# Kernel optimization log

Hardware: AMD Instinct MI355X
Metric: run time of the kernel (lower is better)

Reference implementation:

```python
import jax, jax.numpy as jnp
import numpy as np

EPS = 1e-5
NH = 8   # num_heads
P = 8    # patch_size (local window)

def layernorm(x, g, b):
    m = jnp.mean(x, axis=-1, keepdims=True)
    v = jnp.var(x, axis=-1, keepdims=True)
    return (x - m) * jax.lax.rsqrt(v + EPS) * g + b

def axis_embed(pos, nf):
    # DETR-style interleaved sin/cos along one axis -> (L, nf)
    dim_t = 10000.0 ** (2.0 * (jnp.arange(nf) // 2).astype(jnp.float32) / nf)
    p = pos[:, None] / dim_t
    return jnp.stack([jnp.sin(p[:, 0::2]), jnp.cos(p[:, 1::2])], axis=-1).reshape(pos.shape[0], nf)

def pos_embed_2d(E, H, W):
    # (H, W, E): first half of channels encode y, second half encode x
    half = E // 2
    ye = axis_embed(jnp.arange(1, H + 1, dtype=jnp.float32), half)
    xe = axis_embed(jnp.arange(1, W + 1, dtype=jnp.float32), half)
    return jnp.concatenate([jnp.broadcast_to(ye[:, None, :], (H, W, half)),
                            jnp.broadcast_to(xe[None, :, :], (H, W, half))], axis=-1)

def pos_embed_1d(L, E):
    # standard sinusoidal, (L, 1, E)
    pos = jnp.arange(L, dtype=jnp.float32)[:, None]
    div = jnp.exp(jnp.arange(0, E, 2, dtype=jnp.float32) * (-np.log(10000.0) / E))
    pe = jnp.zeros((L, E), jnp.float32)
    pe = pe.at[:, 0::2].set(jnp.sin(pos * div)).at[:, 1::2].set(jnp.cos(pos * div))
    return pe[:, None, :]

def mha(q, k, v, Wq, bq, Wk, bk, Wv, bv, Wo, bo, nh):
    # q,k,v: (B, L, C)
    B, Lq, C = q.shape
    hd = C // nh
    qh = (q @ Wq + bq).reshape(B, Lq, nh, hd)
    kh = (k @ Wk + bk).reshape(B, -1, nh, hd)
    vh = (v @ Wv + bv).reshape(B, -1, nh, hd)
    att = jax.nn.softmax(jnp.einsum('bqhd,bkhd->bhqk', qh, kh) / np.sqrt(hd).astype(np.float32), axis=-1)
    out = jnp.einsum('bhqk,bkhd->bqhd', att, vh).reshape(B, Lq, C)
    return out @ Wo + bo

def win_part(x):
    # (N,T,H,W,C) -> (N*T*nWin, P*P, C)
    N, T, H, W, C = x.shape
    x = x.reshape(N, T, H // P, P, W // P, P, C).transpose(0, 1, 2, 4, 3, 5, 6)
    return x.reshape(-1, P * P, C)

def forward(x, g1, b1, g2, b2, g3, b3, g4, b4,
            sWq, sbq, sWk, sbk, sWv, sbv, sWo, sbo,
            cW1, cb1, dwk, dwb, cW2, cb2,
            tWq, tbq, tWk, tbk, tWv, tbv, tWo, tbo,
            fW1, fb1, fW2, fb2):
    N, T, H, W, C = x.shape
    sl_pos = jnp.tile(pos_embed_2d(C, P, P), (H // P, W // P, 1))  # (H,W,C)
    tem_pos = pos_embed_1d(T, C)                                   # (T,1,C)

    # --- spatial local windowed MHSA (q=k=norm1(x+pos), v=norm1(x)) ---
    qk = win_part(layernorm(x + sl_pos, g1, b1))
    vv = win_part(layernorm(x, g1, b1))
    attn = mha(qk, qk, vv, sWq, sbq, sWk, sbk, sWv, sbv, sWo, sbo, NH)
    attn = attn.reshape(N, T, H // P, W // P, P, P, C).transpose(0, 1, 2, 4, 3, 5, 6).reshape(N, T, H, W, C)
    x = x + attn

    # --- Conv FFN: linear -> depthwise 3x3 -> GELU -> linear ---
    h = layernorm(x, g2, b2) @ cW1 + cb1
    Ch = h.shape[-1]
    h = h.reshape(N * T, H, W, Ch).transpose(0, 3, 1, 2)  # NCHW
    h = jax.lax.conv_general_dilated(h, dwk, (1, 1), 'SAME', feature_group_count=Ch,
                                     dimension_numbers=('NCHW', 'OIHW', 'NCHW')) + dwb[None, :, None, None]
    h = jax.nn.gelu(h, approximate=False)
    h = h.transpose(0, 2, 3, 1).reshape(N, T, H, W, Ch)
    x = x + (h @ cW2 + cb2)

    # --- temporal MHSA over T, tokens are (n,h,w) positions ---
    xt = x.transpose(1, 0, 2, 3, 4).reshape(T, N * H * W, C)
    xt = layernorm(xt, g3, b3)
    qt = layernorm(xt + tem_pos, g3, b3).transpose(1, 0, 2)  # (B,T,C)
    vt = layernorm(xt, g3, b3).transpose(1, 0, 2)
    xt = xt + mha(qt, qt, vt, tWq, tbq, tWk, tbk, tWv, tbv, tWo, tbo, NH).transpose(1, 0, 2)

    # --- FFN; original does x = x + drop3(x) (no residual, doubles output) ---
    xt = layernorm(xt, g4, b4)
    xt = jax.nn.gelu(xt @ fW1 + fb1, approximate=False) @ fW2 + fb2
    xt = xt + xt
    return xt.reshape(T, N, H, W, C).transpose(1, 0, 2, 3, 4)

def setup_inputs() -> dict:
    key = jax.random.key(0)
    N, T, H, W, C, DFF, HID = 4, 16, 32, 32, 256, 1024, 1024
    ks = iter(jax.random.split(key, 64))
    def w(*s):
        return jax.random.normal(next(ks), s, jnp.float32) * 0.02
    inp = dict(x=jax.random.normal(next(ks), (N, T, H, W, C), jnp.float32))
    for i in ('1', '2', '3', '4'):
        inp['g' + i] = jnp.ones((C,), jnp.float32)
        inp['b' + i] = jnp.zeros((C,), jnp.float32)
    for pfx in ('s', 't'):
        inp.update({pfx + 'Wq': w(C, C), pfx + 'bq': jnp.zeros((C,), jnp.float32),
                    pfx + 'Wk': w(C, C), pfx + 'bk': jnp.zeros((C,), jnp.float32),
                    pfx + 'Wv': w(C, C), pfx + 'bv': jnp.zeros((C,), jnp.float32),
                    pfx + 'Wo': w(C, C), pfx + 'bo': jnp.zeros((C,), jnp.float32)})
    inp.update(cW1=w(C, HID), cb1=jnp.zeros((HID,), jnp.float32),
               dwk=w(HID, 1, 3, 3), dwb=jnp.zeros((HID,), jnp.float32),
               cW2=w(HID, C), cb2=jnp.zeros((C,), jnp.float32))
    inp.update(fW1=w(C, DFF), fb1=jnp.zeros((DFF,), jnp.float32),
               fW2=w(DFF, C), fb2=jnp.zeros((C,), jnp.float32))
    return inp

def reference(x, g1, b1, g2, b2, g3, b3, g4, b4,
              sWq, sbq, sWk, sbk, sWv, sbv, sWo, sbo,
              cW1, cb1, dwk, dwb, cW2, cb2,
              tWq, tbq, tWk, tbk, tWv, tbv, tWo, tbo,
              fW1, fb1, fW2, fb2):
    return forward(x, g1, b1, g2, b2, g3, b3, g4, b4,
                   sWq, sbq, sWk, sbk, sWv, sbv, sWo, sbo,
                   cW1, cb1, dwk, dwb, cW2, cb2,
                   tWq, tbq, tWk, tbk, tWv, tbv, tWo, tbo,
                   fW1, fb1, fW2, fb2)
```

## Files before the change

kernel.cpp:

```cpp
#include <hip/hip_runtime.h>
#include <hip/hip_bf16.h>

typedef unsigned short u16;
typedef unsigned int u32;
typedef __attribute__((ext_vector_type(4))) float f32x4;
typedef __attribute__((ext_vector_type(8))) short s16x8;

static constexpr int Nn = 4, Tt = 16, Hh = 32, Ww = 32, Cc = 256;
static constexpr int Ltok = Nn * Tt * Hh * Ww;

__device__ __forceinline__ float bf2f(u16 v) {
  union { u32 u; float f; } t; t.u = ((u32)v) << 16; return t.f;
}
__device__ __forceinline__ u16 f2bf(float f) {
  union { u32 u; float f; } t; t.f = f;
  return (u16)((t.u + 0x7fffu + ((t.u >> 16) & 1u)) >> 16);
}
__device__ __forceinline__ ushort4 pack4(float a, float b, float c, float d) {
  ushort4 r; r.x = f2bf(a); r.y = f2bf(b); r.z = f2bf(c); r.w = f2bf(d); return r;
}
__device__ __forceinline__ float geluf(float x) {
  return 0.5f * x * (1.0f + erff(x * 0.70710678118654752f));
}
__device__ __forceinline__ float wsum(float v) {
#pragma unroll
  for (int o = 32; o > 0; o >>= 1) v += __shfl_xor(v, o, 64);
  return v;
}
__device__ __forceinline__ void ln_stats(float a0, float a1, float a2, float a3,
                                         float& m, float& inv) {
  float s  = wsum(a0 + a1 + a2 + a3);
  float s2 = wsum(a0 * a0 + a1 * a1 + a2 * a2 + a3 * a3);
  m = s * (1.0f / 256.0f);
  float v = s2 * (1.0f / 256.0f) - m * m;
  inv = rsqrtf(v + 1e-5f);
}
__device__ __forceinline__ void gload16(const u16* g, u16* l) {
  __builtin_amdgcn_global_load_lds(
      (const __attribute__((address_space(1))) void*)g,
      (__attribute__((address_space(3))) void*)l, 16, 0, 0);
}

__global__ __launch_bounds__(256) void k_pos(float* __restrict__ pe2d,
                                             float* __restrict__ pe1d,
                                             float* __restrict__ dwkT,
                                             float* __restrict__ zb,
                                             const float* __restrict__ dwk) {
  int idx = blockIdx.x * 256 + threadIdx.x;
  if (idx < 16384) {
    int y = idx >> 11, r = idx & 2047, x = r >> 8, c = r & 255;
    float pos; int cc;
    if (c < 128) { pos = (float)(y + 1); cc = c; }
    else         { pos = (float)(x + 1); cc = c - 128; }
    float e = (float)(cc & ~1) * (1.0f / 128.0f);
    float v = pos / powf(10000.0f, e);
    pe2d[idx] = (cc & 1) ? cosf(v) : sinf(v);
  } else if (idx < 20480) {
    int i = idx - 16384;
    int t = i >> 8, c = i & 255;
    float e = (float)(c & ~1) * (1.0f / 256.0f);
    float v = (float)t * powf(10000.0f, -e);
    pe1d[i] = (c & 1) ? cosf(v) : sinf(v);
  } else if (idx < 29696) {
    int i = idx - 20480;
    int c = i & 1023, tap = i >> 10;
    dwkT[tap * 1024 + c] = dwk[c * 9 + tap];
  } else if (idx < 30720) {
    zb[idx - 29696] = 0.0f;
  }
}

__global__ __launch_bounds__(256) void k_wprep(
    const float* __restrict__ s0, const float* __restrict__ s1,
    const float* __restrict__ s2, const float* __restrict__ s3,
    const float* __restrict__ s4, const float* __restrict__ s5,
    const float* __restrict__ s6, const float* __restrict__ s7,
    const float* __restrict__ cW1, const float* __restrict__ cW2,
    const float* __restrict__ fW1, const float* __restrict__ fW2,
    u16* __restrict__ WT) {
  __shared__ float Ls[32][33];
  int b = blockIdx.x;
  const float* src; u16* dst; int Kd, Nd, tb;
  if (b < 512) {
    int seg = b >> 6; tb = b & 63; Kd = 256; Nd = 256;
    const float* tab[8] = {s0, s1, s2, s3, s4, s5, s6, s7};
    src = tab[seg]; dst = WT + seg * 65536;
  } else if (b < 768)  { tb = b - 512;  Kd = 256;  Nd = 1024; src = cW1; dst = WT + 524288; }
  else if (b < 1024)   { tb = b - 768;  Kd = 1024; Nd = 256;  src = cW2; dst = WT + 786432; }
  else if (b < 1280)   { tb = b - 1024; Kd = 256;  Nd = 1024; src = fW1; dst = WT + 1048576; }
  else                 { tb = b - 1280; Kd = 1024; Nd = 256;  src = fW2; dst = WT + 1310720; }
  int nt = Nd >> 5;
  int tk = tb / nt, tn = tb % nt;
  int r = threadIdx.x >> 3, c0 = (threadIdx.x & 7) * 4;
  float4 v = *(const float4*)&src[(size_t)(tk * 32 + r) * Nd + tn * 32 + c0];
  Ls[r][c0] = v.x; Ls[r][c0 + 1] = v.y; Ls[r][c0 + 2] = v.z; Ls[r][c0 + 3] = v.w;
  __syncthreads();
  *(ushort4*)&dst[(size_t)(tn * 32 + r) * Kd + tk * 32 + c0] =
      pack4(Ls[c0][r], Ls[c0 + 1][r], Ls[c0 + 2][r], Ls[c0 + 3][r]);
}

__global__ __launch_bounds__(256) void k_ln1(const float* __restrict__ x,
                                             const float* __restrict__ g,
                                             const float* __restrict__ b,
                                             const float* __restrict__ pe2d,
                                             u16* __restrict__ qk,
                                             u16* __restrict__ vv) {
  int l = blockIdx.x * 4 + (threadIdx.x >> 6);
  int lane = threadIdx.x & 63, c0 = lane * 4;
  int idx = l & 1023, hh = idx >> 5, ww = idx & 31;
  float4 xv = *(const float4*)&x[(size_t)l * Cc + c0];
  float4 pv = *(const float4*)&pe2d[(((hh & 7) << 3) | (ww & 7)) * Cc + c0];
  float q0 = xv.x + pv.x, q1 = xv.y + pv.y, q2 = xv.z + pv.z, q3 = xv.w + pv.w;
  float mx, ix, mq, iq;
  ln_stats(xv.x, xv.y, xv.z, xv.w, mx, ix);
  ln_stats(q0, q1, q2, q3, mq, iq);
  float4 gv = *(const float4*)&g[c0];
  float4 bv = *(const float4*)&b[c0];
  *(ushort4*)&qk[(size_t)l * Cc + c0] =
      pack4((q0 - mq) * iq * gv.x + bv.x, (q1 - mq) * iq * gv.y + bv.y,
            (q2 - mq) * iq * gv.z + bv.z, (q3 - mq) * iq * gv.w + bv.w);
  *(ushort4*)&vv[(size_t)l * Cc + c0] =
      pack4((xv.x - mx) * ix * gv.x + bv.x, (xv.y - mx) * ix * gv.y + bv.y,
            (xv.z - mx) * ix * gv.z + bv.z, (xv.w - mx) * ix * gv.w + bv.w);
}

__global__ __launch_bounds__(256) void k_lnb(const u16* __restrict__ x,
                                             const float* __restrict__ g,
                                             const float* __restrict__ b,
                                             u16* __restrict__ out) {
  int l = blockIdx.x * 4 + (threadIdx.x >> 6);
  int lane = threadIdx.x & 63, c0 = lane * 4;
  ushort4 xv4 = *(const ushort4*)&x[(size_t)l * Cc + c0];
  float x0 = bf2f(xv4.x), x1 = bf2f(xv4.y), x2 = bf2f(xv4.z), x3 = bf2f(xv4.w);
  float m, inv;
  ln_stats(x0, x1, x2, x3, m, inv);
  float4 gv = *(const float4*)&g[c0];
  float4 bv = *(const float4*)&b[c0];
  *(ushort4*)&out[(size_t)l * Cc + c0] =
      pack4((x0 - m) * inv * gv.x + bv.x, (x1 - m) * inv * gv.y + bv.y,
            (x2 - m) * inv * gv.z + bv.z, (x3 - m) * inv * gv.w + bv.w);
}

__global__ __launch_bounds__(256) void k_ln3b(const u16* __restrict__ xa,
                                              const float* __restrict__ g,
                                              const float* __restrict__ b,
                                              const float* __restrict__ pe1d,
                                              u16* __restrict__ xt_base,
                                              u16* __restrict__ qt,
                                              u16* __restrict__ vt) {
  int l = blockIdx.x * 4 + (threadIdx.x >> 6);
  int lane = threadIdx.x & 63, c0 = lane * 4;
  ushort4 xv4 = *(const ushort4*)&xa[(size_t)l * Cc + c0];
  float x0 = bf2f(xv4.x), x1 = bf2f(xv4.y), x2 = bf2f(xv4.z), x3 = bf2f(xv4.w);
  float4 gv = *(const float4*)&g[c0];
  float4 bv = *(const float4*)&b[c0];
  float m, inv;
  ln_stats(x0, x1, x2, x3, m, inv);
  float t0 = (x0 - m) * inv * gv.x + bv.x;
  float t1 = (x1 - m) * inv * gv.y + bv.y;
  float t2 = (x2 - m) * inv * gv.z + bv.z;
  float t3 = (x3 - m) * inv * gv.w + bv.w;
  *(ushort4*)&xt_base[(size_t)l * Cc + c0] = pack4(t0, t1, t2, t3);
  float m2, inv2;
  ln_stats(t0, t1, t2, t3, m2, inv2);
  *(ushort4*)&vt[(size_t)l * Cc + c0] =
      pack4((t0 - m2) * inv2 * gv.x + bv.x, (t1 - m2) * inv2 * gv.y + bv.y,
            (t2 - m2) * inv2 * gv.z + bv.z, (t3 - m2) * inv2 * gv.w + bv.w);
  int tt = (l >> 10) & 15;
  float4 pv = *(const float4*)&pe1d[tt * Cc + c0];
  float s0 = t0 + pv.x, s1 = t1 + pv.y, s2 = t2 + pv.z, s3 = t3 + pv.w;
  float m3, inv3;
  ln_stats(s0, s1, s2, s3, m3, inv3);
  *(ushort4*)&qt[(size_t)l * Cc + c0] =
      pack4((s0 - m3) * inv3 * gv.x + bv.x, (s1 - m3) * inv3 * gv.y + bv.y,
            (s2 - m3) * inv3 * gv.z + bv.z, (s3 - m3) * inv3 * gv.w + bv.w);
}

template <int MODE>
__global__ __launch_bounds__(256, 2) void k_sgemm(const u16* __restrict__ A,
                                                  const u16* __restrict__ WT,
                                                  const float* __restrict__ bias,
                                                  const void* __restrict__ res,
                                                  void* __restrict__ out,
                                                  int ldout) {
  __shared__ u16 SMEM[32768];
  const int tid = threadIdx.x;
  const int wave = tid >> 6, lane = tid & 63;
  const int fr = lane & 15, fs = lane >> 4;
  const int r0base = blockIdx.x * 128;
  s16x8 wreg[4][8];
#pragma unroll
  for (int ni = 0; ni < 4; ++ni)
#pragma unroll
    for (int kt = 0; kt < 8; ++kt)
      wreg[ni][kt] = *(const s16x8*)&WT[(size_t)(wave * 64 + ni * 16 + fr) * 256 +
                                        kt * 32 + fs * 8];
  auto stage = [&](int buf, int r0) {
    u16* Ad = SMEM + buf * 8192;
#pragma unroll
    for (int i = 0; i < 4; ++i) {
      int idx = i * 256 + tid;
      int row = idx >> 5, s = idx & 31;
      gload16(A + (size_t)(r0 + row) * 256 + ((s ^ row) << 3), &Ad[idx * 8]);
    }
  };
  float* sc = (float*)(SMEM + 16384) + wave * 2048;
  stage(0, r0base);
  __syncthreads();
#pragma unroll 1
  for (int c = 0; c < 4; ++c) {
    if (c < 3) stage((c + 1) & 1, r0base + (c + 1) * 32);
    const u16* As = SMEM + (c & 1) * 8192;
    f32x4 acc[2][4] = {};
#pragma unroll
    for (int kt = 0; kt < 8; ++kt) {
      s16x8 a0 = *(const s16x8*)&As[(fr * 32 + ((kt * 4 + fs) ^ fr)) * 8];
      s16x8 a1 = *(const s16x8*)&As[((16 + fr) * 32 + ((kt * 4 + fs) ^ (16 + fr))) * 8];
#pragma unroll
      for (int ni = 0; ni < 4; ++ni) {
        acc[0][ni] = __builtin_amdgcn_mfma_f32_16x16x32_bf16(a0, wreg[ni][kt],
                                                             acc[0][ni], 0, 0, 0);
        acc[1][ni] = __builtin_amdgcn_mfma_f32_16x16x32_bf16(a1, wreg[ni][kt],
                                                             acc[1][ni], 0, 0, 0);
      }
    }
    const int r0 = r0base + c * 32;
    if constexpr (MODE == 5) {
      u16* o = (u16*)out;
#pragma unroll
      for (int ni = 0; ni < 4; ++ni) {
        int gc = wave * 64 + ni * 16 + fr;
        float bv = bias[gc];
#pragma unroll
        for (int mi = 0; mi < 2; ++mi) {
          int gr = r0 + mi * 16 + fs * 4;
          *(ushort4*)&o[(size_t)gc * (size_t)Ltok + gr] =
              pack4(acc[mi][ni][0] + bv, acc[mi][ni][1] + bv,
                    acc[mi][ni][2] + bv, acc[mi][ni][3] + bv);
        }
      }
    } else {
#pragma unroll
      for (int mi = 0; mi < 2; ++mi)
#pragma unroll
        for (int ni = 0; ni < 4; ++ni)
#pragma unroll
          for (int r = 0; r < 4; ++r) {
            int row = mi * 16 + fs * 4 + r;
            int col = ni * 16 + fr;
            sc[row * 64 + (col ^ ((row & 7) << 3))] = acc[mi][ni][r];
          }
#pragma unroll
      for (int p = 0; p < 8; ++p) {
        int row = p * 4 + (lane >> 4);
        int c4 = (lane & 15) * 4;
        f32x4 v4 = *(const f32x4*)&sc[row * 64 + (c4 ^ ((row & 7) << 3))];
        int gr = r0 + row;
        int gc = wave * 64 + c4;
        float4 bv4 = *(const float4*)&bias[gc];
        float v[4] = {v4[0] + bv4.x, v4[1] + bv4.y, v4[2] + bv4.z, v4[3] + bv4.w};
        size_t o = (size_t)gr * (size_t)ldout + gc;
        if constexpr (MODE == 1) {
#pragma unroll
          for (int j = 0; j < 4; ++j) v[j] = geluf(v[j]);
        }
        if constexpr (MODE == 3) {
          ushort4 r4 = *(const ushort4*)&((const u16*)res)[(size_t)gr * 256 + gc];
          v[0] += bf2f(r4.x); v[1] += bf2f(r4.y); v[2] += bf2f(r4.z); v[3] += bf2f(r4.w);
        }
        if constexpr (MODE == 7) {
          float4 r4 = *(const float4*)&((const float*)res)[(size_t)gr * 256 + gc];
          v[0] += r4.x; v[1] += r4.y; v[2] += r4.z; v[3] += r4.w;
        }
        *(ushort4*)&((u16*)out)[o] = pack4(v[0], v[1], v[2], v[3]);
      }
    }
    __syncthreads();
  }
}

template <int MODE>
__global__ __launch_bounds__(256, 2) void k_m2(const u16* __restrict__ A,
                                               const u16* __restrict__ BT, int ldbt,
                                               const float* __restrict__ bias,
                                               const void* __restrict__ res,
                                               void* __restrict__ out, int K) {
  __shared__ u16 SMEM[16384];
  const int tid = threadIdx.x;
  const int wave = tid >> 6, lane = tid & 63;
  const int fr = lane & 15, fs = lane >> 4;
  const int m0 = blockIdx.x * 128, n0 = blockIdx.y * 64;
  const int wm = wave >> 1, wn = wave & 1;
  f32x4 acc[4][2] = {};

  auto stage = [&](int buf, int k0) {
    u16* Ad = SMEM + buf * 6144;
    u16* Bd = Ad + 4096;
#pragma unroll
    for (int i = 0; i < 2; ++i) {
      int idx = i * 256 + tid;
      int row = idx >> 2, s = idx & 3;
      gload16(A + (size_t)(m0 + row) * K + k0 + ((s ^ (row & 3)) << 3), &Ad[idx * 8]);
    }
    {
      int row = tid >> 2, s = tid & 3;
      gload16(BT + (size_t)(n0 + row) * ldbt + k0 + ((s ^ (row & 3)) << 3),
              &Bd[tid * 8]);
    }
  };
  auto compute = [&](int buf) {
    const u16* As = SMEM + buf * 6144;
    const u16* Bs = As + 4096;
    s16x8 af[4], bfr[2];
#pragma unroll
    for (int i = 0; i < 4; ++i) {
      int ra = wm * 64 + i * 16 + fr;
      af[i] = *(const s16x8*)&As[ra * 32 + ((fs ^ (ra & 3)) << 3)];
    }
#pragma unroll
    for (int j = 0; j < 2; ++j) {
      int rb = wn * 32 + j * 16 + fr;
      bfr[j] = *(const s16x8*)&Bs[rb * 32 + ((fs ^ (rb & 3)) << 3)];
    }
#pragma unroll
    for (int mi = 0; mi < 4; ++mi)
#pragma unroll
      for (int nj = 0; nj < 2; ++nj)
        acc[mi][nj] = __builtin_amdgcn_mfma_f32_16x16x32_bf16(af[mi], bfr[nj],
                                                              acc[mi][nj], 0, 0, 0);
  };

  stage(0, 0);
  __syncthreads();
  const int nt = K >> 5;
  int cur = 0;
  for (int t = 0; t < nt; ++t) {
    if (t < nt - 1) stage(cur ^ 1, (t + 1) << 5);
    compute(cur);
    __syncthreads();
    cur ^= 1;
  }
  float* Wl = (float*)SMEM + wave * 2048;
#pragma unroll
  for (int nj = 0; nj < 2; ++nj)
#pragma unroll
    for (int mi = 0; mi < 4; ++mi)
#pragma unroll
      for (int r = 0; r < 4; ++r) {
        int row = mi * 16 + fs * 4 + r;
        int col = nj * 16 + fr;
        Wl[row * 32 + (col ^ ((row & 7) << 2))] = acc[mi][nj][r];
      }
#pragma unroll
  for (int p = 0; p < 8; ++p) {
    int row = p * 8 + (lane >> 3);
    int c4 = (lane & 7) * 4;
    f32x4 v4 = *(const f32x4*)&Wl[row * 32 + (c4 ^ ((row & 7) << 2))];
    int gr = m0 + wm * 64 + row;
    int gc = n0 + wn * 32 + c4;
    float4 bv4 = *(const float4*)&bias[gc];
    float v[4] = {v4[0] + bv4.x, v4[1] + bv4.y, v4[2] + bv4.z, v4[3] + bv4.w};
    size_t o = (size_t)gr * 256 + gc;
    if constexpr (MODE == 3) {
      ushort4 r4 = *(const ushort4*)&((const u16*)res)[o];
      v[0] += bf2f(r4.x); v[1] += bf2f(r4.y); v[2] += bf2f(r4.z); v[3] += bf2f(r4.w);
      *(ushort4*)&((u16*)out)[o] = pack4(v[0], v[1], v[2], v[3]);
    } else {
      *(float4*)&((float*)out)[o] =
          make_float4(v[0] * 2.0f, v[1] * 2.0f, v[2] * 2.0f, v[3] * 2.0f);
    }
  }
}

__global__ __launch_bounds__(256) void k_sattn2(const u16* __restrict__ Q,
                                                const u16* __restrict__ Kb,
                                                const u16* __restrict__ VT,
                                                u16* __restrict__ ctx) {
  __shared__ u16 P_lds[4][4096];
  const int tid = threadIdx.x;
  const int wave = tid >> 6, lane = tid & 63;
  const int fr = lane & 15, fs = lane >> 4;
  const int wi = blockIdx.x >> 1;
  const int head = (blockIdx.x & 1) * 4 + wave;
  const int ft = wi >> 4, wy = (wi >> 2) & 3, wx = wi & 3;
  const int base = ft * 1024 + wy * 256 + wx * 8;
  const float scale = 0.17677669529663688f;
  const int ch = head * 32 + fs * 8;
  s16x8 ka[4], qb[4];
#pragma unroll
  for (int t4 = 0; t4 < 4; ++t4) {
    int tok = base + (2 * t4 + (fr >> 3)) * 32 + (fr & 7);
    ka[t4] = *(const s16x8*)&Kb[(size_t)tok * 256 + ch];
    qb[t4] = *(const s16x8*)&Q[(size_t)tok * 256 + ch];
  }
  f32x4 s[4][4] = {};
#pragma unroll
  for (int kt = 0; kt < 4; ++kt)
#pragma unroll
    for (int qt = 0; qt < 4; ++qt)
      s[kt][qt] = __builtin_amdgcn_mfma_f32_16x16x32_bf16(ka[kt], qb[qt], s[kt][qt], 0, 0, 0);
  u16* pw = P_lds[wave];
#pragma unroll
  for (int qt = 0; qt < 4; ++qt) {
    float m = -1e30f;
#pragma unroll
    for (int kt = 0; kt < 4; ++kt)
#pragma unroll
      for (int r = 0; r < 4; ++r) m = fmaxf(m, s[kt][qt][r]);
    m = fmaxf(m, __shfl_xor(m, 16, 64));
    m = fmaxf(m, __shfl_xor(m, 32, 64));
    m *= scale;
    float e[4][4];
    float sum = 0.f;
#pragma unroll
    for (int kt = 0; kt < 4; ++kt)
#pragma unroll
      for (int r = 0; r < 4; ++r) {
        e[kt][r] = __expf(s[kt][qt][r] * scale - m);
        sum += e[kt][r];
      }
    sum += __shfl_xor(sum, 16, 64);
    sum += __shfl_xor(sum, 32, 64);
    float il = 1.0f / sum;
    int q = qt * 16 + fr;
    int rowb = q * 128, sw = (q & 7) << 4;
#pragma unroll
    for (int kt = 0; kt < 4; ++kt)
      *(ushort4*)((char*)pw + ((rowb + kt * 32 + fs * 8) ^ sw)) =
          pack4(e[kt][0] * il, e[kt][1] * il, e[kt][2] * il, e[kt][3] * il);
  }
  f32x4 o[4][2] = {};
#pragma unroll
  for (int ks = 0; ks < 2; ++ks) {
    s16x8 vb[2];
#pragma unroll
    for (int nt = 0; nt < 2; ++nt) {
      int d = head * 32 + nt * 16 + fr;
      int tok = base + (ks * 4 + fs) * 32;
      vb[nt] = *(const s16x8*)&VT[(size_t)d * (size_t)Ltok + tok];
    }
#pragma unroll
    for (int qt = 0; qt < 4; ++qt) {
      int q = qt * 16 + fr;
      s16x8 pa = *(const s16x8*)((char*)pw +
                                 ((q * 128 + ks * 64 + fs * 16) ^ ((q & 7) << 4)));
#pragma unroll
      for (int nt = 0; nt < 2; ++nt)
        o[qt][nt] = __builtin_amdgcn_mfma_f32_16x16x32_bf16(pa, vb[nt], o[qt][nt], 0, 0, 0);
    }
  }
#pragma unroll
  for (int qt = 0; qt < 4; ++qt)
#pragma unroll
    for (int r = 0; r < 4; ++r) {
      int q = qt * 16 + fs * 4 + r;
      int tok = base + (q >> 3) * 32 + (q & 7);
#pragma unroll
      for (int nt = 0; nt < 2; ++nt)
        ctx[(size_t)tok * 256 + head * 32 + nt * 16 + fr] = f2bf(o[qt][nt][r]);
    }
}

__global__ __launch_bounds__(256) void k_tattn2(const u16* __restrict__ Q,
                                                const u16* __restrict__ Kb,
                                                const u16* __restrict__ V,
                                                u16* __restrict__ ctx) {
  __shared__ u16 Vs[16 * 256];
  const int tid = threadIdx.x;
  const int b = blockIdx.x;
  const int n = b >> 10, hw = b & 1023;
  const int tok0 = n * 16384 + hw;
#pragma unroll
  for (int i = 0; i < 2; ++i) {
    int chunk = tid * 2 + i;
    int row = chunk >> 5, c8 = (chunk & 31) * 8;
    *(uint4*)&Vs[row * 256 + c8] =
        *(const uint4*)&V[(size_t)(tok0 + row * 1024) * 256 + c8];
  }
  __syncthreads();
  const int wave = tid >> 6, lane = tid & 63;
  const int fr = lane & 15, fs = lane >> 4;
  const float scale = 0.17677669529663688f;
#pragma unroll
  for (int hg = 0; hg < 2; ++hg) {
    int head = wave + hg * 4;
    int ch = head * 32 + fs * 8;
    size_t go = (size_t)(tok0 + fr * 1024) * 256 + ch;
    s16x8 ka = *(const s16x8*)&Kb[go];
    s16x8 qb = *(const s16x8*)&Q[go];
    f32x4 s = {0.f, 0.f, 0.f, 0.f};
    s = __builtin_amdgcn_mfma_f32_16x16x32_bf16(ka, qb, s, 0, 0, 0);
    float m = fmaxf(fmaxf(s[0], s[1]), fmaxf(s[2], s[3]));
    m = fmaxf(m, __shfl_xor(m, 16, 64));
    m = fmaxf(m, __shfl_xor(m, 32, 64));
    m *= scale;
    float e0 = __expf(s[0] * scale - m), e1 = __expf(s[1] * scale - m);
    float e2 = __expf(s[2] * scale - m), e3 = __expf(s[3] * scale - m);
    float sum = e0 + e1 + e2 + e3;
    sum += __shfl_xor(sum, 16, 64);
    sum += __shfl_xor(sum, 32, 64);
    float il = 1.0f / sum;
    e0 *= il; e1 *= il; e2 *= il; e3 *= il;
    float o[8] = {};
#pragma unroll
    for (int kb = 0; kb < 4; ++kb) {
      int src = kb * 16 + fr;
      float p0 = __shfl(e0, src, 64);
      float p1 = __shfl(e1, src, 64);
      float p2 = __shfl(e2, src, 64);
      float p3 = __shfl(e3, src, 64);
#pragma unroll
      for (int r = 0; r < 4; ++r) {
        float p = r == 0 ? p0 : (r == 1 ? p1 : (r == 2 ? p2 : p3));
        uint4 vv = *(const uint4*)&Vs[(kb * 4 + r) * 256 + ch];
        const u16* vp = (const u16*)&vv;
#pragma unroll
        for (int u = 0; u < 8; ++u) o[u] = fmaf(p, bf2f(vp[u]), o[u]);
      }
    }
    size_t co = (size_t)(tok0 + fr * 1024) * 256 + ch;
    *(ushort4*)&ctx[co] = pack4(o[0], o[1], o[2], o[3]);
    *(ushort4*)&ctx[co + 4] = pack4(o[4], o[5], o[6], o[7]);
  }
}

__global__ __launch_bounds__(256) void k_dwconv(const u16* __restrict__ Hin,
                                                const float* __restrict__ dwkT,
                                                const float* __restrict__ dwb,
                                                int ch0, int oco,
                                                u16* __restrict__ Hout) {
  int flat = blockIdx.x * 256 + threadIdx.x;
  int l = flat >> 5, cg = flat & 31, c0 = cg * 8, tc0 = ch0 + c0;
  int frame = l >> 10, idx = l & 1023, hh = idx >> 5, ww = idx & 31;
  float acc[8];
  *(float4*)&acc[0] = *(const float4*)&dwb[tc0];
  *(float4*)&acc[4] = *(const float4*)&dwb[tc0 + 4];
#pragma unroll
  for (int ky = -1; ky <= 1; ++ky) {
    int h2 = hh + ky;
    if (h2 < 0 || h2 >= 32) continue;
#pragma unroll
    for (int kx = -1; kx <= 1; ++kx) {
      int w2 = ww + kx;
      if (w2 < 0 || w2 >= 32) continue;
      int ln = frame * 1024 + h2 * 32 + w2;
      uint4 hv = *(const uint4*)&Hin[(size_t)ln * 256 + c0];
      const u16* hp = (const u16*)&hv;
      int tap = (ky + 1) * 3 + (kx + 1);
      float wk[8];
      *(float4*)&wk[0] = *(const float4*)&dwkT[tap * 1024 + tc0];
      *(float4*)&wk[4] = *(const float4*)&dwkT[tap * 1024 + tc0 + 4];
#pragma unroll
      for (int u = 0; u < 8; ++u) acc[u] = fmaf(bf2f(hp[u]), wk[u], acc[u]);
    }
  }
  size_t ob = (size_t)l * 512 + oco + c0;
  *(ushort4*)&Hout[ob] = pack4(geluf(acc[0]), geluf(acc[1]), geluf(acc[2]), geluf(acc[3]));
  *(ushort4*)&Hout[ob + 4] = pack4(geluf(acc[4]), geluf(acc[5]), geluf(acc[6]), geluf(acc[7]));
}

extern "C" void kernel_launch(void* const* d_in, const int* in_sizes, int n_in,
                              void* d_out, int out_size, void* d_ws, size_t ws_size,
                              hipStream_t stream) {
  (void)in_sizes; (void)n_in; (void)out_size; (void)ws_size;
  const float* x   = (const float*)d_in[0];
  const float* g1  = (const float*)d_in[1];  const float* b1  = (const float*)d_in[2];
  const float* g2  = (const float*)d_in[3];  const float* b2  = (const float*)d_in[4];
  const float* g3  = (const float*)d_in[5];  const float* b3  = (const float*)d_in[6];
  const float* g4  = (const float*)d_in[7];  const float* b4  = (const float*)d_in[8];
  const float* sWq = (const float*)d_in[9];  const float* sbq = (const float*)d_in[10];
  const float* sWk = (const float*)d_in[11]; const float* sbk = (const float*)d_in[12];
  const float* sWv = (const float*)d_in[13]; const float* sbv = (const float*)d_in[14];
  const float* sWo = (const float*)d_in[15]; const float* sbo = (const float*)d_in[16];
  const float* tWq = (const float*)d_in[17]; const float* tbq = (const float*)d_in[18];
  const float* tWk = (const float*)d_in[19]; const float* tbk = (const float*)d_in[20];
  const float* tWv = (const float*)d_in[21]; const float* tbv = (const float*)d_in[22];
  const float* tWo = (const float*)d_in[23]; const float* tbo = (const float*)d_in[24];
  const float* cW1 = (const float*)d_in[25]; const float* cb1 = (const float*)d_in[26];
  const float* dwk = (const float*)d_in[27]; const float* dwb = (const float*)d_in[28];
  const float* cW2 = (const float*)d_in[29]; const float* cb2 = (const float*)d_in[30];
  const float* fW1 = (const float*)d_in[31]; const float* fb1 = (const float*)d_in[32];
  const float* fW2 = (const float*)d_in[33]; const float* fb2 = (const float*)d_in[34];

  char* ws = (char*)d_ws;
  const size_t MB = 1ull << 20;
  float* PE2D = (float*)(ws);
  float* PE1D = (float*)(ws + (64 << 10));
  float* DWKT = (float*)(ws + (80 << 10));
  float* ZB   = (float*)(ws + (116 << 10));
  u16*   WT   = (u16*)(ws + (128 << 10));
  u16* XA  = (u16*)(ws + 4 * MB);
  u16* X1  = (u16*)(ws + 4 * MB);
  u16* B1  = (u16*)(ws + 68 * MB);
  u16* B2  = (u16*)(ws + 100 * MB);
  u16* B3  = (u16*)(ws + 132 * MB);
  u16* B4  = (u16*)(ws + 164 * MB);
  u16* F1  = (u16*)(ws + 4 * MB);
  u16* H1q = B2;
  u16* H2h = B3;

  u16* sWqT = WT;               u16* sWkT = WT + 65536;
  u16* sWvT = WT + 2 * 65536;   u16* sWoT = WT + 3 * 65536;
  u16* tWqT = WT + 4 * 65536;   u16* tWkT = WT + 5 * 65536;
  u16* tWvT = WT + 6 * 65536;   u16* tWoT = WT + 7 * 65536;
  u16* cW1T = WT + 524288;      u16* cW2T = WT + 786432;
  u16* fW1T = WT + 1048576;     u16* fW2T = WT + 1310720;

  dim3 blk(256);
  dim3 gLN(Ltok / 4);
  dim3 gS(512);
  dim3 gM2(512, 4);

  k_pos<<<dim3(120), blk, 0, stream>>>(PE2D, PE1D, DWKT, ZB, dwk);
  k_wprep<<<dim3(1536), blk, 0, stream>>>(sWq, sWk, sWv, sWo, tWq, tWk, tWv, tWo,
                                          cW1, cW2, fW1, fW2, WT);
  k_ln1<<<gLN, blk, 0, stream>>>(x, g1, b1, PE2D, B1, B2);
  k_sgemm<5><<<gS, blk, 0, stream>>>(B2, sWvT, sbv, nullptr, B3, 0);
  k_sgemm<0><<<gS, blk, 0, stream>>>(B1, sWqT, sbq, nullptr, B2, 256);
  k_sgemm<0><<<gS, blk, 0, stream>>>(B1, sWkT, sbk, nullptr, B4, 256);
  k_sattn2<<<dim3(2048), blk, 0, stream>>>(B2, B4, B3, B1);
  k_sgemm<7><<<gS, blk, 0, stream>>>(B1, sWoT, sbo, x, XA, 256);
  k_lnb<<<gLN, blk, 0, stream>>>(XA, g2, b2, B1);
  for (int h = 0; h < 2; ++h) {
    for (int qq = 0; qq < 2; ++qq) {
      int q = h * 2 + qq;
      k_sgemm<0><<<gS, blk, 0, stream>>>(B1, cW1T + q * 65536, cb1 + q * 256,
                                         nullptr, H1q, 256);
      k_dwconv<<<dim3(Ltok * 32 / 256), blk, 0, stream>>>(H1q, DWKT, dwb,
                                                          q * 256, qq * 256, H2h);
    }
    k_m2<3><<<gM2, blk, 0, stream>>>(H2h, cW2T + h * 512, 1024,
                                     h ? cb2 : ZB, XA, XA, 512);
  }
  k_ln3b<<<gLN, blk, 0, stream>>>(XA, g3, b3, PE1D, B1, B2, B3);
  k_sgemm<0><<<gS, blk, 0, stream>>>(B3, tWvT, tbv, nullptr, B4, 256);
  k_sgemm<0><<<gS, blk, 0, stream>>>(B2, tWqT, tbq, nullptr, X1, 256);
  k_sgemm<0><<<gS, blk, 0, stream>>>(B2, tWkT, tbk, nullptr, B3, 256);
  k_tattn2<<<dim3(4096), blk, 0, stream>>>(X1, B3, B4, B2);
  k_sgemm<3><<<gS, blk, 0, stream>>>(B2, tWoT, tbo, B1, B3, 256);
  k_lnb<<<gLN, blk, 0, stream>>>(B3, g4, b4, B4);
  for (int q = 0; q < 4; ++q)
    k_sgemm<1><<<gS, blk, 0, stream>>>(B4, fW1T + q * 65536, fb1 + q * 256,
                                       nullptr, F1 + q * 256, 1024);
  k_m2<4><<<gM2, blk, 0, stream>>>(F1, fW2T, 1024, fb2, nullptr,
                                   (float*)d_out, 1024);
}
```

Before: 792.8 us.

## Widen k_m2 tile to 128x128 and stage transposed MODE 5 stores through LDS

```diff
diff --git a/kernel.cpp b/kernel.cpp
--- a/kernel.cpp
+++ b/kernel.cpp
@@ -205,6 +205,7 @@
     }
   };
   float* sc = (float*)(SMEM + 16384) + wave * 2048;
+  u16* sc2 = SMEM + 16384 + wave * 2048;
   stage(0, r0base);
   __syncthreads();
 #pragma unroll 1
@@ -229,15 +230,23 @@
       u16* o = (u16*)out;
 #pragma unroll
       for (int ni = 0; ni < 4; ++ni) {
-        int gc = wave * 64 + ni * 16 + fr;
-        float bv = bias[gc];
-#pragma unroll
-        for (int mi = 0; mi < 2; ++mi) {
-          int gr = r0 + mi * 16 + fs * 4;
-          *(ushort4*)&o[(size_t)gc * (size_t)Ltok + gr] =
-              pack4(acc[mi][ni][0] + bv, acc[mi][ni][1] + bv,
-                    acc[mi][ni][2] + bv, acc[mi][ni][3] + bv);
-        }
+        float bv = bias[wave * 64 + ni * 16 + fr];
+#pragma unroll
+        for (int mi = 0; mi < 2; ++mi)
+#pragma unroll
+          for (int r = 0; r < 4; ++r) {
+            int row = mi * 16 + fs * 4 + r;
+            int col = ni * 16 + fr;
+            sc2[col * 32 + row] = f2bf(acc[mi][ni][r] + bv);
+          }
+      }
+#pragma unroll
+      for (int p = 0; p < 4; ++p) {
+        int gcl = p * 16 + (lane >> 2);
+        int sub = lane & 3;
+        uint4 u = *(const uint4*)&sc2[gcl * 32 + sub * 8];
+        int gc = wave * 64 + gcl;
+        *(uint4*)&o[(size_t)gc * (size_t)Ltok + r0 + sub * 8] = u;
       }
     } else {
 #pragma unroll
@@ -289,45 +298,40 @@
   const int tid = threadIdx.x;
   const int wave = tid >> 6, lane = tid & 63;
   const int fr = lane & 15, fs = lane >> 4;
-  const int m0 = blockIdx.x * 128, n0 = blockIdx.y * 64;
+  const int bid = blockIdx.x;
+  const int m0 = (bid >> 1) * 128, n0 = (bid & 1) * 128;
   const int wm = wave >> 1, wn = wave & 1;
-  f32x4 acc[4][2] = {};
+  f32x4 acc[4][4] = {};
 
   auto stage = [&](int buf, int k0) {
-    u16* Ad = SMEM + buf * 6144;
+    u16* Ad = SMEM + buf * 8192;
     u16* Bd = Ad + 4096;
 #pragma unroll
     for (int i = 0; i < 2; ++i) {
       int idx = i * 256 + tid;
       int row = idx >> 2, s = idx & 3;
       gload16(A + (size_t)(m0 + row) * K + k0 + ((s ^ (row & 3)) << 3), &Ad[idx * 8]);
-    }
-    {
-      int row = tid >> 2, s = tid & 3;
       gload16(BT + (size_t)(n0 + row) * ldbt + k0 + ((s ^ (row & 3)) << 3),
-              &Bd[tid * 8]);
+              &Bd[idx * 8]);
     }
   };
   auto compute = [&](int buf) {
-    const u16* As = SMEM + buf * 6144;
+    const u16* As = SMEM + buf * 8192;
     const u16* Bs = As + 4096;
-    s16x8 af[4], bfr[2];
+    s16x8 af[4], bfr[4];
 #pragma unroll
     for (int i = 0; i < 4; ++i) {
       int ra = wm * 64 + i * 16 + fr;
       af[i] = *(const s16x8*)&As[ra * 32 + ((fs ^ (ra & 3)) << 3)];
-    }
-#pragma unroll
-    for (int j = 0; j < 2; ++j) {
-      int rb = wn * 32 + j * 16 + fr;
-      bfr[j] = *(const s16x8*)&Bs[rb * 32 + ((fs ^ (rb & 3)) << 3)];
+      int rb = wn * 64 + i * 16 + fr;
+      bfr[i] = *(const s16x8*)&Bs[rb * 32 + ((fs ^ (rb & 3)) << 3)];
     }
 #pragma unroll
     for (int mi = 0; mi < 4; ++mi)
 #pragma unroll
-      for (int nj = 0; nj < 2; ++nj)
-        acc[mi][nj] = __builtin_amdgcn_mfma_f32_16x16x32_bf16(af[mi], bfr[nj],
-                                                              acc[mi][nj], 0, 0, 0);
+      for (int ni = 0; ni < 4; ++ni)
+        acc[mi][ni] = __builtin_amdgcn_mfma_f32_16x16x32_bf16(af[mi], bfr[ni],
+                                                              acc[mi][ni], 0, 0, 0);
   };
 
   stage(0, 0);
@@ -342,33 +346,39 @@
   }
   float* Wl = (float*)SMEM + wave * 2048;
 #pragma unroll
-  for (int nj = 0; nj < 2; ++nj)
+  for (int nh = 0; nh < 2; ++nh) {
 #pragma unroll
     for (int mi = 0; mi < 4; ++mi)
 #pragma unroll
-      for (int r = 0; r < 4; ++r) {
-        int row = mi * 16 + fs * 4 + r;
-        int col = nj * 16 + fr;
-        Wl[row * 32 + (col ^ ((row & 7) << 2))] = acc[mi][nj][r];
-      }
-#pragma unroll
-  for (int p = 0; p < 8; ++p) {
-    int row = p * 8 + (lane >> 3);
-    int c4 = (lane & 7) * 4;
-    f32x4 v4 = *(const f32x4*)&Wl[row * 32 + (c4 ^ ((row & 7) << 2))];
-    int gr = m0 + wm * 64 + row;
-    int gc = n0 + wn * 32 + c4;
-    float4 bv4 = *(const float4*)&bias[gc];
-    float v[4] = {v4[0] + bv4.x, v4[1] + bv4.y, v4[2] + bv4.z, v4[3] + bv4.w};
-    size_t o = (size_t)gr * 256 + gc;
-    if constexpr (MODE == 3) {
-      ushort4 r4 = *(const ushort4*)&((const u16*)res)[o];
-      v[0] += bf2f(r4.x); v[1] += bf2f(r4.y); v[2] += bf2f(r4.z); v[3] += bf2f(r4.w);
-      *(ushort4*)&((u16*)out)[o] = pack4(v[0], v[1], v[2], v[3]);
-    } else {
-      *(float4*)&((float*)out)[o] =
-          make_float4(v[0] * 2.0f, v[1] * 2.0f, v[2] * 2.0f, v[3] * 2.0f);
-    }
+      for (int nq = 0; nq < 2; ++nq) {
+        int ni = nh * 2 + nq;
+#pragma unroll
+        for (int r = 0; r < 4; ++r) {
+          int row = mi * 16 + fs * 4 + r;
+          int col = nq * 16 + fr;
+          Wl[row * 32 + (col ^ ((row & 7) << 2))] = acc[mi][ni][r];
+        }
+      }
+#pragma unroll
+    for (int p = 0; p < 8; ++p) {
+      int row = p * 8 + (lane >> 3);
+      int c4 = (lane & 7) * 4;
+      f32x4 v4 = *(const f32x4*)&Wl[row * 32 + (c4 ^ ((row & 7) << 2))];
+      int gr = m0 + wm * 64 + row;
+      int gc = n0 + wn * 64 + nh * 32 + c4;
+      float4 bv4 = *(const float4*)&bias[gc];
+      float v[4] = {v4[0] + bv4.x, v4[1] + bv4.y, v4[2] + bv4.z, v4[3] + bv4.w};
+      size_t o = (size_t)gr * 256 + gc;
+      if constexpr (MODE == 3) {
+        ushort4 r4 = *(const ushort4*)&((const u16*)res)[o];
+        v[0] += bf2f(r4.x); v[1] += bf2f(r4.y); v[2] += bf2f(r4.z); v[3] += bf2f(r4.w);
+        *(ushort4*)&((u16*)out)[o] = pack4(v[0], v[1], v[2], v[3]);
+      } else {
+        *(float4*)&((float*)out)[o] =
+            make_float4(v[0] * 2.0f, v[1] * 2.0f, v[2] * 2.0f, v[3] * 2.0f);
+      }
+    }
+    __syncthreads();
   }
 }
 
@@ -609,7 +619,7 @@
   dim3 blk(256);
   dim3 gLN(Ltok / 4);
   dim3 gS(512);
-  dim3 gM2(512, 4);
+  dim3 gM2(1024);
 
   k_pos<<<dim3(120), blk, 0, stream>>>(PE2D, PE1D, DWKT, ZB, dwk);
   k_wprep<<<dim3(1536), blk, 0, stream>>>(sWq, sWk, sWv, sWo, tWq, tWk, tWv, tWo,
```

Measured after the change: 766.7 us. -3.3%, faster.
